# Kernel tuning notes

Hardware: AMD Instinct MI355X
Metric: run time of the kernel (lower is better)

The kernel has to match this reference:

```python
import math
import jax, jax.numpy as jnp
import numpy as np

R_MIN, R_MAX, R_BINS = 0.0, 10.0, 64
Z_MIN, Z_MAX, Z_BINS = -2.0, 2.0, 64
DR = (R_MAX - R_MIN) / R_BINS
DZ = (Z_MAX - Z_MIN) / Z_BINS
N = 16777216


def setup_inputs() -> dict:
    key = jax.random.key(0)
    k1, k2 = jax.random.split(key)
    positions = jax.random.normal(k1, (N, 3), dtype=jnp.float32)
    masses = jax.random.uniform(k2, (N,), dtype=jnp.float32)
    return {"positions": positions, "masses": masses}


def _volume():
    redge = R_MIN + jnp.arange(R_BINS + 1, dtype=jnp.float32) * DR
    area = math.pi * (redge[1:] ** 2 - redge[:-1] ** 2)  # [R_BINS]
    return area * DZ


def reference(positions, masses):
    r_cyl = jnp.sqrt(positions[:, 0] ** 2 + positions[:, 1] ** 2)
    i = jnp.floor((r_cyl - R_MIN) / DR).astype(jnp.int32)
    j = jnp.floor((positions[:, 2] - Z_MIN) / DZ).astype(jnp.int32)
    gd = (i >= 0) & (i < R_BINS) & (j >= 0) & (j < Z_BINS)
    flat = jnp.where(gd, i * Z_BINS + j, 0)
    w = jnp.where(gd, masses, 0.0)
    mass_in_bin = jnp.zeros((R_BINS * Z_BINS,), dtype=masses.dtype).at[flat].add(w)
    mass_in_bin = mass_in_bin.reshape(R_BINS, Z_BINS)
    surface_density = mass_in_bin / _volume()[:, None]
    return surface_density
```

## Files before the change

### kernel.cpp

```cpp
#include <hip/hip_runtime.h>
#include <math.h>

#define R_BINS 64
#define Z_BINS 64
#define NBINS (R_BINS * Z_BINS)
#define BLOCK 512
#define WAVES_PER_BLOCK 8
#define GRID 1024

static constexpr float DR     = 10.0f / 64.0f;
static constexpr float DZ     = 4.0f  / 64.0f;
static constexpr float INV_DR = 6.4f;
static constexpr float INV_DZ = 16.0f;

__global__ __launch_bounds__(BLOCK) void hist_kernel(const float4* __restrict__ pos4,
                                                     const float* __restrict__ mass,
                                                     float* __restrict__ gbins,
                                                     int nchunks) {
    __shared__ float lbins[NBINS];
    __shared__ float4 stage[WAVES_PER_BLOCK][192];

    const int lane = threadIdx.x & 63;
    const int w    = threadIdx.x >> 6;

    for (int b = threadIdx.x; b < NBINS; b += BLOCK) lbins[b] = 0.0f;
    __syncthreads();

    const int totalWaves = gridDim.x * WAVES_PER_BLOCK;
    float* s = (float*)&stage[w][0];

    for (int c = blockIdx.x * WAVES_PER_BLOCK + w; c < nchunks; c += totalWaves) {
        const float4* pb = pos4 + (size_t)192 * c;
        const float4 f0 = pb[lane];
        const float4 f1 = pb[64 + lane];
        const float4 f2 = pb[128 + lane];

        const float* mb = mass + (size_t)256 * c;
        const float m0 = mb[lane];
        const float m1 = mb[64 + lane];
        const float m2 = mb[128 + lane];
        const float m3 = mb[192 + lane];

        stage[w][lane]       = f0;
        stage[w][64 + lane]  = f1;
        stage[w][128 + lane] = f2;
        __asm__ volatile("s_waitcnt lgkmcnt(0)" ::: "memory");
        __builtin_amdgcn_wave_barrier();

        const float ms[4] = {m0, m1, m2, m3};
#pragma unroll
        for (int k = 0; k < 4; ++k) {
            const int p = 64 * k + lane;
            const float x = s[3 * p];
            const float y = s[3 * p + 1];
            const float z = s[3 * p + 2];
            const float r = sqrtf(x * x + y * y);
            const int i = (int)(r * INV_DR);
            const int j = (int)floorf((z + 2.0f) * INV_DZ);
            if (i < R_BINS && (unsigned)j < (unsigned)Z_BINS) {
                atomicAdd(&lbins[i * Z_BINS + j], ms[k]);
            }
        }
        __asm__ volatile("" ::: "memory");
        __builtin_amdgcn_wave_barrier();
    }

    __syncthreads();
    for (int b = threadIdx.x; b < NBINS; b += BLOCK) {
        const float v = lbins[b];
        if (v != 0.0f) atomicAdd(&gbins[b], v);
    }
}

__global__ void tail_kernel(const float* __restrict__ pos,
                            const float* __restrict__ mass,
                            float* __restrict__ gbins,
                            int start, int n) {
    const int t = start + blockIdx.x * blockDim.x + threadIdx.x;
    if (t < n) {
        const float x = pos[3 * t], y = pos[3 * t + 1], z = pos[3 * t + 2];
        const float r = sqrtf(x * x + y * y);
        const int i = (int)(r * INV_DR);
        const int j = (int)floorf((z + 2.0f) * INV_DZ);
        if (i < R_BINS && (unsigned)j < (unsigned)Z_BINS) {
            atomicAdd(&gbins[i * Z_BINS + j], mass[t]);
        }
    }
}

__global__ __launch_bounds__(256) void finalize_kernel(const float* __restrict__ gbins,
                                                       float* __restrict__ out) {
    const int idx = blockIdx.x * blockDim.x + threadIdx.x;
    if (idx < NBINS) {
        const int i = idx / Z_BINS;
        const float r0 = (float)i * DR;
        const float r1 = (float)(i + 1) * DR;
        const float area = (float)M_PI * (r1 * r1 - r0 * r0);
        out[idx] = gbins[idx] / (area * DZ);
    }
}

extern "C" void kernel_launch(void* const* d_in, const int* in_sizes, int n_in,
                              void* d_out, int out_size, void* d_ws, size_t ws_size,
                              hipStream_t stream) {
    const float* positions = (const float*)d_in[0];
    const float* masses    = (const float*)d_in[1];
    float* out   = (float*)d_out;
    float* gbins = (float*)d_ws;

    const int n = in_sizes[1];
    const int nchunks = n / 256;
    const int rem = n - nchunks * 256;

    hipMemsetAsync(gbins, 0, NBINS * sizeof(float), stream);

    hist_kernel<<<GRID, BLOCK, 0, stream>>>((const float4*)positions, masses,
                                            gbins, nchunks);
    if (rem > 0) {
        tail_kernel<<<(rem + 255) / 256, 256, 0, stream>>>(positions, masses,
                                                           gbins, nchunks * 256, n);
    }
    finalize_kernel<<<(NBINS + 255) / 256, 256, 0, stream>>>(gbins, out);
}
```

Measured before the change: 326.4 us.

## Replace global atomic merge with per-block partial histograms and a reduction kernel

```diff
diff --git a/kernel.cpp b/kernel.cpp
--- a/kernel.cpp
+++ b/kernel.cpp
@@ -7,6 +7,10 @@
 #define BLOCK 512
 #define WAVES_PER_BLOCK 8
 #define GRID 1024
+#define NPART GRID
+
+#define RBLOCK 512
+#define RGRID (NBINS / 64)
 
 static constexpr float DR     = 10.0f / 64.0f;
 static constexpr float DZ     = 4.0f  / 64.0f;
@@ -15,7 +19,7 @@
 
 __global__ __launch_bounds__(BLOCK) void hist_kernel(const float4* __restrict__ pos4,
                                                      const float* __restrict__ mass,
-                                                     float* __restrict__ gbins,
+                                                     float* __restrict__ partials,
                                                      int nchunks) {
     __shared__ float lbins[NBINS];
     __shared__ float4 stage[WAVES_PER_BLOCK][192];
@@ -66,15 +70,15 @@
     }
 
     __syncthreads();
-    for (int b = threadIdx.x; b < NBINS; b += BLOCK) {
-        const float v = lbins[b];
-        if (v != 0.0f) atomicAdd(&gbins[b], v);
-    }
+    float4* p4 = (float4*)(partials + (size_t)blockIdx.x * NBINS);
+    const float4* l4 = (const float4*)lbins;
+    p4[threadIdx.x]         = l4[threadIdx.x];
+    p4[BLOCK + threadIdx.x] = l4[BLOCK + threadIdx.x];
 }
 
 __global__ void tail_kernel(const float* __restrict__ pos,
                             const float* __restrict__ mass,
-                            float* __restrict__ gbins,
+                            float* __restrict__ partials,
                             int start, int n) {
     const int t = start + blockIdx.x * blockDim.x + threadIdx.x;
     if (t < n) {
@@ -83,20 +87,38 @@
         const int i = (int)(r * INV_DR);
         const int j = (int)floorf((z + 2.0f) * INV_DZ);
         if (i < R_BINS && (unsigned)j < (unsigned)Z_BINS) {
-            atomicAdd(&gbins[i * Z_BINS + j], mass[t]);
+            atomicAdd(&partials[i * Z_BINS + j], mass[t]);
         }
     }
 }
 
-__global__ __launch_bounds__(256) void finalize_kernel(const float* __restrict__ gbins,
-                                                       float* __restrict__ out) {
-    const int idx = blockIdx.x * blockDim.x + threadIdx.x;
-    if (idx < NBINS) {
-        const int i = idx / Z_BINS;
+__global__ __launch_bounds__(RBLOCK) void reduce_finalize(const float* __restrict__ partials,
+                                                          float* __restrict__ out) {
+    __shared__ float red[RBLOCK];
+    const int t   = threadIdx.x;
+    const int bl  = t & 63;
+    const int grp = t >> 6;
+    const int bin = blockIdx.x * 64 + bl;
+
+    float a0 = 0.0f, a1 = 0.0f, a2 = 0.0f, a3 = 0.0f;
+    for (int sb = grp; sb < NPART; sb += 32) {
+        a0 += partials[(size_t)(sb)      * NBINS + bin];
+        a1 += partials[(size_t)(sb + 8)  * NBINS + bin];
+        a2 += partials[(size_t)(sb + 16) * NBINS + bin];
+        a3 += partials[(size_t)(sb + 24) * NBINS + bin];
+    }
+    red[t] = (a0 + a1) + (a2 + a3);
+    __syncthreads();
+
+    if (t < 64) {
+        float acc = 0.0f;
+#pragma unroll
+        for (int g = 0; g < 8; ++g) acc += red[g * 64 + bl];
+        const int i = bin >> 6;
         const float r0 = (float)i * DR;
         const float r1 = (float)(i + 1) * DR;
         const float area = (float)M_PI * (r1 * r1 - r0 * r0);
-        out[idx] = gbins[idx] / (area * DZ);
+        out[bin] = acc / (area * DZ);
     }
 }
 
@@ -105,20 +127,18 @@
                               hipStream_t stream) {
     const float* positions = (const float*)d_in[0];
     const float* masses    = (const float*)d_in[1];
-    float* out   = (float*)d_out;
-    float* gbins = (float*)d_ws;
+    float* out      = (float*)d_out;
+    float* partials = (float*)d_ws;
 
     const int n = in_sizes[1];
     const int nchunks = n / 256;
     const int rem = n - nchunks * 256;
 
-    hipMemsetAsync(gbins, 0, NBINS * sizeof(float), stream);
-
     hist_kernel<<<GRID, BLOCK, 0, stream>>>((const float4*)positions, masses,
-                                            gbins, nchunks);
+                                            partials, nchunks);
     if (rem > 0) {
         tail_kernel<<<(rem + 255) / 256, 256, 0, stream>>>(positions, masses,
-                                                           gbins, nchunks * 256, n);
+                                                           partials, nchunks * 256, n);
     }
-    finalize_kernel<<<(NBINS + 255) / 256, 256, 0, stream>>>(gbins, out);
+    reduce_finalize<<<RGRID, RBLOCK, 0, stream>>>(partials, out);
 }
```

Measured after the change: 335.9 us. 2.9% more time.

## Drop LDS staging; each thread loads 4 particles as 3 float4 plus float4 mass

Applied to the files above, without the earlier changes.

```diff
diff --git a/kernel.cpp b/kernel.cpp
--- a/kernel.cpp
+++ b/kernel.cpp
@@ -5,7 +5,6 @@
 #define Z_BINS 64
 #define NBINS (R_BINS * Z_BINS)
 #define BLOCK 512
-#define WAVES_PER_BLOCK 8
 #define GRID 1024
 
 static constexpr float DR     = 10.0f / 64.0f;
@@ -13,56 +12,62 @@
 static constexpr float INV_DR = 6.4f;
 static constexpr float INV_DZ = 16.0f;
 
+__device__ __forceinline__ void bin1(float x, float y, float z, float m,
+                                     float* __restrict__ lbins) {
+    const float r = sqrtf(x * x + y * y);
+    const int i = (int)(r * INV_DR);
+    const int j = (int)floorf((z + 2.0f) * INV_DZ);
+    if (i < R_BINS && (unsigned)j < (unsigned)Z_BINS) {
+        atomicAdd(&lbins[i * Z_BINS + j], m);
+    }
+}
+
 __global__ __launch_bounds__(BLOCK) void hist_kernel(const float4* __restrict__ pos4,
-                                                     const float* __restrict__ mass,
+                                                     const float4* __restrict__ mass4,
                                                      float* __restrict__ gbins,
-                                                     int nchunks) {
+                                                     int ngroups) {
     __shared__ float lbins[NBINS];
-    __shared__ float4 stage[WAVES_PER_BLOCK][192];
-
-    const int lane = threadIdx.x & 63;
-    const int w    = threadIdx.x >> 6;
 
     for (int b = threadIdx.x; b < NBINS; b += BLOCK) lbins[b] = 0.0f;
     __syncthreads();
 
-    const int totalWaves = gridDim.x * WAVES_PER_BLOCK;
-    float* s = (float*)&stage[w][0];
+    const int gpb   = (ngroups + GRID - 1) / GRID;
+    const int gbeg  = blockIdx.x * gpb;
+    const int gend  = min(gbeg + gpb, ngroups);
 
-    for (int c = blockIdx.x * WAVES_PER_BLOCK + w; c < nchunks; c += totalWaves) {
-        const float4* pb = pos4 + (size_t)192 * c;
-        const float4 f0 = pb[lane];
-        const float4 f1 = pb[64 + lane];
-        const float4 f2 = pb[128 + lane];
+    int g = gbeg + threadIdx.x;
+    for (; g + BLOCK < gend; g += 2 * BLOCK) {
+        const size_t ga = (size_t)g * 3;
+        const size_t gb = (size_t)(g + BLOCK) * 3;
+        const float4 a0 = pos4[ga];
+        const float4 a1 = pos4[ga + 1];
+        const float4 a2 = pos4[ga + 2];
+        const float4 b0 = pos4[gb];
+        const float4 b1 = pos4[gb + 1];
+        const float4 b2 = pos4[gb + 2];
+        const float4 am = mass4[g];
+        const float4 bm = mass4[g + BLOCK];
 
-        const float* mb = mass + (size_t)256 * c;
-        const float m0 = mb[lane];
-        const float m1 = mb[64 + lane];
-        const float m2 = mb[128 + lane];
-        const float m3 = mb[192 + lane];
+        bin1(a0.x, a0.y, a0.z, am.x, lbins);
+        bin1(a0.w, a1.x, a1.y, am.y, lbins);
+        bin1(a1.z, a1.w, a2.x, am.z, lbins);
+        bin1(a2.y, a2.z, a2.w, am.w, lbins);
 
-        stage[w][lane]       = f0;
-        stage[w][64 + lane]  = f1;
-        stage[w][128 + lane] = f2;
-        __asm__ volatile("s_waitcnt lgkmcnt(0)" ::: "memory");
-        __builtin_amdgcn_wave_barrier();
-
-        const float ms[4] = {m0, m1, m2, m3};
-#pragma unroll
-        for (int k = 0; k < 4; ++k) {
-            const int p = 64 * k + lane;
-            const float x = s[3 * p];
-            const float y = s[3 * p + 1];
-            const float z = s[3 * p + 2];
-            const float r = sqrtf(x * x + y * y);
-            const int i = (int)(r * INV_DR);
-            const int j = (int)floorf((z + 2.0f) * INV_DZ);
-            if (i < R_BINS && (unsigned)j < (unsigned)Z_BINS) {
-                atomicAdd(&lbins[i * Z_BINS + j], ms[k]);
-            }
-        }
-        __asm__ volatile("" ::: "memory");
-        __builtin_amdgcn_wave_barrier();
+        bin1(b0.x, b0.y, b0.z, bm.x, lbins);
+        bin1(b0.w, b1.x, b1.y, bm.y, lbins);
+        bin1(b1.z, b1.w, b2.x, bm.z, lbins);
+        bin1(b2.y, b2.z, b2.w, bm.w, lbins);
+    }
+    for (; g < gend; g += BLOCK) {
+        const size_t ga = (size_t)g * 3;
+        const float4 a0 = pos4[ga];
+        const float4 a1 = pos4[ga + 1];
+        const float4 a2 = pos4[ga + 2];
+        const float4 am = mass4[g];
+        bin1(a0.x, a0.y, a0.z, am.x, lbins);
+        bin1(a0.w, a1.x, a1.y, am.y, lbins);
+        bin1(a1.z, a1.w, a2.x, am.z, lbins);
+        bin1(a2.y, a2.z, a2.w, am.w, lbins);
     }
 
     __syncthreads();
@@ -109,16 +114,17 @@
     float* gbins = (float*)d_ws;
 
     const int n = in_sizes[1];
-    const int nchunks = n / 256;
-    const int rem = n - nchunks * 256;
+    const int ngroups = n / 4;
+    const int rem = n - ngroups * 4;
 
     hipMemsetAsync(gbins, 0, NBINS * sizeof(float), stream);
 
-    hist_kernel<<<GRID, BLOCK, 0, stream>>>((const float4*)positions, masses,
-                                            gbins, nchunks);
+    hist_kernel<<<GRID, BLOCK, 0, stream>>>((const float4*)positions,
+                                            (const float4*)masses,
+                                            gbins, ngroups);
     if (rem > 0) {
         tail_kernel<<<(rem + 255) / 256, 256, 0, stream>>>(positions, masses,
-                                                           gbins, nchunks * 256, n);
+                                                           gbins, ngroups * 4, n);
     }
     finalize_kernel<<<(NBINS + 255) / 256, 256, 0, stream>>>(gbins, out);
 }
```

Measured after the change: 327.5 us. About the same (+0.3%).

## Double-buffer per-wave chunks via direct global-to-LDS loads with contiguous ranges

Applied to the files above, without the earlier changes.

```diff
diff --git a/kernel.cpp b/kernel.cpp
--- a/kernel.cpp
+++ b/kernel.cpp
@@ -6,19 +6,35 @@
 #define NBINS (R_BINS * Z_BINS)
 #define BLOCK 512
 #define WAVES_PER_BLOCK 8
-#define GRID 1024
+#define GRID 512
 
 static constexpr float DR     = 10.0f / 64.0f;
 static constexpr float DZ     = 4.0f  / 64.0f;
 static constexpr float INV_DR = 6.4f;
 static constexpr float INV_DZ = 16.0f;
 
+__device__ __forceinline__ void bin1(float x, float y, float z, float m,
+                                     float* __restrict__ lbins) {
+    const float r = sqrtf(x * x + y * y);
+    const int i = (int)(r * INV_DR);
+    const int j = (int)floorf((z + 2.0f) * INV_DZ);
+    if (i < R_BINS && (unsigned)j < (unsigned)Z_BINS) {
+        atomicAdd(&lbins[i * Z_BINS + j], m);
+    }
+}
+
+__device__ __forceinline__ void g2l16(const void* g, void* l) {
+    __builtin_amdgcn_global_load_lds(
+        (const __attribute__((address_space(1))) unsigned int*)g,
+        (__attribute__((address_space(3))) unsigned int*)l, 16, 0, 0);
+}
+
 __global__ __launch_bounds__(BLOCK) void hist_kernel(const float4* __restrict__ pos4,
-                                                     const float* __restrict__ mass,
+                                                     const float4* __restrict__ mass4,
                                                      float* __restrict__ gbins,
                                                      int nchunks) {
-    __shared__ float lbins[NBINS];
-    __shared__ float4 stage[WAVES_PER_BLOCK][192];
+    __shared__ float  lbins[NBINS];
+    __shared__ float4 stage[WAVES_PER_BLOCK][2][256];
 
     const int lane = threadIdx.x & 63;
     const int w    = threadIdx.x >> 6;
@@ -26,42 +42,42 @@
     for (int b = threadIdx.x; b < NBINS; b += BLOCK) lbins[b] = 0.0f;
     __syncthreads();
 
-    const int totalWaves = gridDim.x * WAVES_PER_BLOCK;
-    float* s = (float*)&stage[w][0];
+    const int totalWaves = GRID * WAVES_PER_BLOCK;
+    const int wid  = blockIdx.x * WAVES_PER_BLOCK + w;
+    const int per  = (nchunks + totalWaves - 1) / totalWaves;
+    const int c0   = wid * per;
+    const int c1   = min(c0 + per, nchunks);
 
-    for (int c = blockIdx.x * WAVES_PER_BLOCK + w; c < nchunks; c += totalWaves) {
-        const float4* pb = pos4 + (size_t)192 * c;
-        const float4 f0 = pb[lane];
-        const float4 f1 = pb[64 + lane];
-        const float4 f2 = pb[128 + lane];
+    if (c0 < c1) {
+        const float4* pb = pos4 + (size_t)192 * c0 + lane;
+        float4* d = &stage[w][c0 & 1][0];
+        g2l16(pb,       d);
+        g2l16(pb + 64,  d + 64);
+        g2l16(pb + 128, d + 128);
+        g2l16(mass4 + (size_t)64 * c0 + lane, d + 192);
+    }
 
-        const float* mb = mass + (size_t)256 * c;
-        const float m0 = mb[lane];
-        const float m1 = mb[64 + lane];
-        const float m2 = mb[128 + lane];
-        const float m3 = mb[192 + lane];
-
-        stage[w][lane]       = f0;
-        stage[w][64 + lane]  = f1;
-        stage[w][128 + lane] = f2;
-        __asm__ volatile("s_waitcnt lgkmcnt(0)" ::: "memory");
+    for (int c = c0; c < c1; ++c) {
+        if (c + 1 < c1) {
+            const float4* pb = pos4 + (size_t)192 * (c + 1) + lane;
+            float4* d = &stage[w][(c + 1) & 1][0];
+            g2l16(pb,       d);
+            g2l16(pb + 64,  d + 64);
+            g2l16(pb + 128, d + 128);
+            g2l16(mass4 + (size_t)64 * (c + 1) + lane, d + 192);
+            __asm__ volatile("s_waitcnt vmcnt(4)" ::: "memory");
+        } else {
+            __asm__ volatile("s_waitcnt vmcnt(0)" ::: "memory");
+        }
+        __builtin_amdgcn_sched_barrier(0);
         __builtin_amdgcn_wave_barrier();
 
-        const float ms[4] = {m0, m1, m2, m3};
+        const float* s = (const float*)&stage[w][c & 1][0];
 #pragma unroll
         for (int k = 0; k < 4; ++k) {
-            const int p = 64 * k + lane;
-            const float x = s[3 * p];
-            const float y = s[3 * p + 1];
-            const float z = s[3 * p + 2];
-            const float r = sqrtf(x * x + y * y);
-            const int i = (int)(r * INV_DR);
-            const int j = (int)floorf((z + 2.0f) * INV_DZ);
-            if (i < R_BINS && (unsigned)j < (unsigned)Z_BINS) {
-                atomicAdd(&lbins[i * Z_BINS + j], ms[k]);
-            }
+            const int p = (k << 6) + lane;
+            bin1(s[3 * p], s[3 * p + 1], s[3 * p + 2], s[768 + p], lbins);
         }
-        __asm__ volatile("" ::: "memory");
         __builtin_amdgcn_wave_barrier();
     }
 
@@ -114,7 +130,8 @@
 
     hipMemsetAsync(gbins, 0, NBINS * sizeof(float), stream);
 
-    hist_kernel<<<GRID, BLOCK, 0, stream>>>((const float4*)positions, masses,
+    hist_kernel<<<GRID, BLOCK, 0, stream>>>((const float4*)positions,
+                                            (const float4*)masses,
                                             gbins, nchunks);
     if (rem > 0) {
         tail_kernel<<<(rem + 255) / 256, 256, 0, stream>>>(positions, masses,
```

After: 332.9 us. Within noise of the previous version (+2.0%).
